# Kernel optimization log

Measured on AMD Instinct MI355X. Metric: run time of the kernel, lower is better.

Reference implementation:

```python
import jax, jax.numpy as jnp
import numpy as np

H = 256; EMB = 256; MAX_POS = 20; NBOND = 4; ATOM = 40
DEPTH_T = 5; DEPTH_G = 5
NT, MT = 8000, 16000      # tree nodes / tree messages
NA, MA = 25000, 50000     # atoms / bond messages
NB = 6; NC = 12; NROOT = 256
VC, VI = 5000, 15000      # cluster / inter vocab sizes

FLOAT_KEYS = ("E_c","E_i","Wc_w","Wc_b","Wi_w","Wi_b","Wroot_w","Wroot_b",
  "t_Wo_w","t_Wo_b","t_Wz_w","t_Wz_b","t_Wr_w","t_Ur_w","t_Ur_b","t_Wh_w","t_Wh_b",
  "i_Wo_w","i_Wo_b","i_Wz_w","i_Wz_b","i_Wr_w","i_Ur_w","i_Ur_b","i_Wh_w","i_Wh_b",
  "g_Wo_w","g_Wo_b","g_Wz_w","g_Wz_b","g_Wr_w","g_Ur_w","g_Ur_b","g_Wh_w","g_Wh_b")
INT_KEYS = ("t_fnode","t_fmess","t_agraph","t_bgraph","t_cgraph",
            "g_fnode","g_fmess","g_agraph","g_bgraph","roots")

def _gru(fmess, bgraph, Wz_w, Wz_b, Wr_w, Ur_w, Ur_b, Wh_w, Wh_b, depth):
    # depth-iterated GRU message passing; row 0 of h is padding (kept at zero).
    M, F = fmess.shape
    Hs = Wz_w.shape[1]
    mask = jnp.ones((M, 1), fmess.dtype).at[0, 0].set(0.0)
    # loop-invariant input projections (W_z/W_h split along concat axis)
    fz = fmess @ Wz_w[:F] + Wz_b
    fr = fmess @ Wr_w
    fh = fmess @ Wh_w[:F] + Wh_b
    Wz_h, Wh_h = Wz_w[F:], Wh_w[F:]
    def step(h, _):
        h_nei = h[bgraph]                       # [M, B, H] irregular gather
        sum_h = h_nei.sum(1)
        z = jax.nn.sigmoid(fz + sum_h @ Wz_h)
        r = jax.nn.sigmoid(fr[:, None, :] + h_nei @ Ur_w + Ur_b)
        sum_gh = (r * h_nei).sum(1)
        pre_h = jnp.tanh(fh + sum_gh @ Wh_h)
        h_new = ((1.0 - z) * sum_h + z * pre_h) * mask
        return h_new, None
    h0 = jnp.zeros((M, Hs), fmess.dtype)
    h, _ = jax.lax.scan(step, h0, None, length=depth)
    return h

def _mpn(fnode, fmess, agraph, bgraph, p, depth):
    h = _gru(fmess, bgraph, p["Wz_w"], p["Wz_b"], p["Wr_w"], p["Ur_w"], p["Ur_b"], p["Wh_w"], p["Wh_b"], depth)
    nei = h[agraph].sum(1)                      # index_select_ND + sum
    nh = jax.nn.relu(jnp.concatenate([fnode, nei], 1) @ p["Wo_w"] + p["Wo_b"])
    return nh.at[0].set(0.0), h                 # zero padding row (mask)

def _enc_params(fl, pre):
    return {k: fl[pre + k] for k in ("Wo_w","Wo_b","Wz_w","Wz_b","Wr_w","Ur_w","Ur_b","Wh_w","Wh_b")}

def _forward(fl, it):
    E_pos = jnp.eye(MAX_POS, dtype=jnp.float32)
    E_a = jnp.eye(ATOM, dtype=jnp.float32)
    E_b = jnp.eye(NBOND, dtype=jnp.float32)
    t_fnode, t_fmess = it["t_fnode"], it["t_fmess"]
    g_fnode, g_fmess = it["g_fnode"], it["g_fmess"]
    # ---- embed_graph + graph_encoder ----
    g_hnode = E_a[g_fnode]                                           # [NA, ATOM] one-hot
    g_hmess = jnp.concatenate([g_hnode[g_fmess[:, 0]], E_b[g_fmess[:, 2]], E_pos[g_fmess[:, 3]]], 1)
    hatom, _ = _mpn(g_hnode, g_hmess, it["g_agraph"], it["g_bgraph"], _enc_params(fl, "g_"), DEPTH_G)
    # ---- embed_inter + inter_encoder ----
    fin = fl["E_i"][t_fnode[:, 1]]
    hn = hatom[it["t_cgraph"]].sum(1)                                # cluster <- atoms
    hn = jax.nn.relu(jnp.concatenate([fin, hn], 1) @ fl["Wi_w"] + fl["Wi_b"])
    hm = jnp.concatenate([hn[t_fmess[:, 0]], E_pos[t_fmess[:, 2]]], 1)
    hinter, _ = _mpn(hn, hm, it["t_agraph"], it["t_bgraph"], _enc_params(fl, "i_"), DEPTH_T)
    # ---- embed_tree + tree_encoder ----
    fin = fl["E_c"][t_fnode[:, 0]]
    hn = jax.nn.relu(jnp.concatenate([fin, hinter], 1) @ fl["Wc_w"] + fl["Wc_b"])
    hm = jnp.concatenate([hn[t_fmess[:, 0]], E_pos[t_fmess[:, 2]]], 1)
    htree, h_msg = _mpn(hn, hm, it["t_agraph"], it["t_bgraph"], _enc_params(fl, "t_"), DEPTH_T)
    # ---- embed_root: uses pre-encoder node embedding hn and message states h_msg ----
    r = it["roots"]
    nei = h_msg[it["t_agraph"][r]].sum(1)
    hroot = jnp.tanh(jnp.concatenate([hn[r], nei], 1) @ fl["Wroot_w"] + fl["Wroot_b"])
    return hroot, htree, hinter, hatom

def setup_inputs() -> dict:
    ki = iter(jax.random.split(jax.random.key(0), 80))
    def nk():
        return next(ki)
    ri = jax.random.randint
    rn = lambda shape: 0.08 * jax.random.normal(nk(), shape, jnp.float32)
    inp = {}
    inp["t_fnode"] = ri(nk(), (NT, 2), 0, VC)
    inp["t_fmess"] = jnp.stack([ri(nk(), (MT,), 0, NT), ri(nk(), (MT,), 0, NT), ri(nk(), (MT,), 0, MAX_POS)], 1)
    inp["t_agraph"] = ri(nk(), (NT, NB), 0, MT)
    inp["t_bgraph"] = ri(nk(), (MT, NB), 0, MT)
    inp["t_cgraph"] = ri(nk(), (NT, NC), 0, NA)
    inp["g_fnode"] = ri(nk(), (NA,), 0, ATOM)
    inp["g_fmess"] = jnp.stack([ri(nk(), (MA,), 0, NA), ri(nk(), (MA,), 0, NA), ri(nk(), (MA,), 0, NBOND), ri(nk(), (MA,), 0, MAX_POS)], 1)
    inp["g_agraph"] = ri(nk(), (NA, NB), 0, MA)
    inp["g_bgraph"] = ri(nk(), (MA, NB), 0, MA)
    inp["roots"] = ri(nk(), (NROOT,), 0, NT)
    inp["E_c"] = rn((VC, EMB)); inp["E_i"] = rn((VI, EMB))
    inp["Wc_w"] = rn((EMB + H, H)); inp["Wc_b"] = rn((H,))
    inp["Wi_w"] = rn((EMB + H, H)); inp["Wi_b"] = rn((H,))
    inp["Wroot_w"] = rn((2 * H, H)); inp["Wroot_b"] = rn((H,))
    for pre, in_sz, nf in (("t_", H + MAX_POS, H), ("i_", H + MAX_POS, H), ("g_", ATOM + NBOND + MAX_POS, ATOM)):
        inp[pre + "Wo_w"] = rn((nf + H, H)); inp[pre + "Wo_b"] = rn((H,))
        inp[pre + "Wz_w"] = rn((in_sz + H, H)); inp[pre + "Wz_b"] = rn((H,))
        inp[pre + "Wr_w"] = rn((in_sz, H))
        inp[pre + "Ur_w"] = rn((H, H)); inp[pre + "Ur_b"] = rn((H,))
        inp[pre + "Wh_w"] = rn((in_sz + H, H)); inp[pre + "Wh_b"] = rn((H,))
    return inp

def reference(E_c, E_i, Wc_w, Wc_b, Wi_w, Wi_b, Wroot_w, Wroot_b,
              t_Wo_w, t_Wo_b, t_Wz_w, t_Wz_b, t_Wr_w, t_Ur_w, t_Ur_b, t_Wh_w, t_Wh_b,
              i_Wo_w, i_Wo_b, i_Wz_w, i_Wz_b, i_Wr_w, i_Ur_w, i_Ur_b, i_Wh_w, i_Wh_b,
              g_Wo_w, g_Wo_b, g_Wz_w, g_Wz_b, g_Wr_w, g_Ur_w, g_Ur_b, g_Wh_w, g_Wh_b,
              t_fnode, t_fmess, t_agraph, t_bgraph, t_cgraph,
              g_fnode, g_fmess, g_agraph, g_bgraph, roots):
    a = dict(locals())
    fl = {k: a[k] for k in FLOAT_KEYS}
    it = {k: a[k] for k in INT_KEYS}
    return _forward(fl, it)
```

## Files before the change

kernel.cpp:

```cpp
#include <hip/hip_runtime.h>
#include <hip/hip_bf16.h>
#include <math.h>

typedef __hip_bfloat16 bf16;
typedef __attribute__((ext_vector_type(8))) short  bf16x8;
typedef __attribute__((ext_vector_type(4))) float  f32x4;

#define NT_ 8000
#define MT_ 16000
#define NA_ 25000
#define MA_ 50000
#define NROOT_ 256

struct Feat {
  const float* dtab; const int* didx; int dstride;
  const float* otab;
  const int* oidx0; int os0; int oo0;
  const int* oidx1; int os1; int oo1;
  const int* oidx2; int os2; int oo2;
  const float* bias;
};

__device__ __forceinline__ float rcpf_(float x){ return __builtin_amdgcn_rcpf(x); }
__device__ __forceinline__ float sigm(float x){ return rcpf_(1.0f + __expf(-x)); }
__device__ __forceinline__ float tanh_f(float x){
  float t = __expf(2.0f*x);
  return 1.0f - 2.0f*rcpf_(t + 1.0f);
}

__device__ __forceinline__ float ubf(unsigned int u){ union{unsigned int i; float f;} x; x.i = u<<16; return x.f; }
__device__ __forceinline__ unsigned int pack2bf(float a, float b){
  bf16 x = __float2bfloat16(a), y = __float2bfloat16(b);
  unsigned short ux = *(unsigned short*)&x, uy = *(unsigned short*)&y;
  return (unsigned int)ux | ((unsigned int)uy<<16);
}
__device__ __forceinline__ short f2bf_s(float f){
  bf16 b = __float2bfloat16(f);
  return *(short*)&b;
}
__device__ __forceinline__ float bfs2f(short s){ return ubf((unsigned short)s); }

__device__ __forceinline__ void acc4(float4& v, const float* p){
  float4 t = *(const float4*)p;
  v.x+=t.x; v.y+=t.y; v.z+=t.z; v.w+=t.w;
}
__device__ __forceinline__ float4 feat_eval4(const Feat& f, int m, int n){
  float4 v = make_float4(0,0,0,0);
  if (f.bias) acc4(v, f.bias + n);
  if (f.dtab) acc4(v, f.dtab + (size_t)f.didx[(size_t)m*f.dstride]*256 + n);
  if (f.otab){
    acc4(v, f.otab + (size_t)(f.oidx0[(size_t)m*f.os0]+f.oo0)*256 + n);
    if (f.oidx1) acc4(v, f.otab + (size_t)(f.oidx1[(size_t)m*f.os1]+f.oo1)*256 + n);
    if (f.oidx2) acc4(v, f.otab + (size_t)(f.oidx2[(size_t)m*f.os2]+f.oo2)*256 + n);
  }
  return v;
}
__device__ __forceinline__ float feat_eval(const Feat& f, int m, int n){
  float v = 0.0f;
  if (f.bias) v += f.bias[n];
  if (f.dtab) v += f.dtab[(size_t)f.didx[(size_t)m*f.dstride]*256 + n];
  if (f.otab){
    v += f.otab[((size_t)(f.oidx0[(size_t)m*f.os0]+f.oo0))*256 + n];
    if (f.oidx1) v += f.otab[((size_t)(f.oidx1[(size_t)m*f.os1]+f.oo1))*256 + n];
    if (f.oidx2) v += f.otab[((size_t)(f.oidx2[(size_t)m*f.os2]+f.oo2))*256 + n];
  }
  return v;
}

__global__ void k_aidx(const int* __restrict__ g_fnode, const int* __restrict__ g_fmess,
                       int* __restrict__ aidx, int M){
  int m = blockIdx.x*blockDim.x + threadIdx.x;
  if (m<M) aidx[m] = g_fnode[g_fmess[(size_t)m*4]];
}

struct SJob { const float* src; short* dst; int nrow; int pad; };
struct SJobs { SJob j[26]; };
__global__ void k_splitw_b(SJobs js){
  SJob jb = js.j[blockIdx.y];
  int idx = blockIdx.x*256 + threadIdx.x;
  if (idx >= jb.nrow*256) return;
  int k = idx>>8, n = idx&255;
  float w = jb.src[idx];
  int base = (((k>>5)*16 + (n>>4))<<10) + (((n&15) + (((k>>3)&3)<<4))<<4) + (k&7);
  short h = f2bf_s(w);
  jb.dst[base]   = h;
  jb.dst[base+8] = f2bf_s(w - bfs2f(h));
}

__global__ void k_gsum4(const float* __restrict__ src, const int* __restrict__ idx,
                        const int* __restrict__ rowsel, int J, int istride,
                        float* __restrict__ dst, int M){
  int wid = (blockIdx.x<<2) + (threadIdx.x>>6);
  if (wid>=M) return;
  int c = (threadIdx.x&63)<<2;
  int r = rowsel ? rowsel[wid] : wid;
  float4 s = make_float4(0,0,0,0);
  for (int j=0;j<J;j++){
    int id = idx[(size_t)r*istride+j];
    acc4(s, src + (size_t)id*256 + c);
  }
  *(float4*)(dst + (size_t)wid*256 + c) = s;
}

__device__ __forceinline__ void build_a(const float* p, bf16x8& hi, bf16x8& lo){
  float4 v0 = *(const float4*)p;
  float4 v1 = *(const float4*)(p+4);
  float vv[8]={v0.x,v0.y,v0.z,v0.w,v1.x,v1.y,v1.z,v1.w};
  #pragma unroll
  for (int j=0;j<8;j++){
    short h = f2bf_s(vv[j]);
    hi[j]=h;
    lo[j]=f2bf_s(vv[j]-bfs2f(h));
  }
}

#define MFMA __builtin_amdgcn_mfma_f32_16x16x32_bf16
#define PRIO_HI __builtin_amdgcn_s_setprio(1)
#define PRIO_LO __builtin_amdgcn_s_setprio(0)

__global__ __launch_bounds__(256)
void mfma_mm(const float* __restrict__ A, const short* __restrict__ Bp,
             float* __restrict__ outf, int M)
{
  const int tid=threadIdx.x, lane=tid&63, wc=tid>>6;
  const int rbase = blockIdx.x<<5;
  const int r0 = rbase + (lane&15), r1 = r0 + 16;
  const int koff = (lane>>4)<<3;
  f32x4 zero = {0.f,0.f,0.f,0.f};
  f32x4 acc[2][4];
  #pragma unroll
  for (int rf=0;rf<2;rf++)
    #pragma unroll
    for (int t=0;t<4;t++) acc[rf][t]=zero;

  PRIO_HI;
  for (int kc=0;kc<8;kc++){
    bf16x8 a0h={0,0,0,0,0,0,0,0}, a0l=a0h, a1h=a0h, a1l=a0h;
    if (r0<M) build_a(A + (size_t)r0*256 + kc*32 + koff, a0h, a0l);
    if (r1<M) build_a(A + (size_t)r1*256 + kc*32 + koff, a1h, a1l);
    #pragma unroll
    for (int t=0;t<4;t++){
      const short* p = Bp + (((kc<<4)+(wc<<2)+t)<<10) + (lane<<4);
      bf16x8 bh = *(const bf16x8*)p;
      bf16x8 bl = *(const bf16x8*)(p+8);
      acc[0][t]=MFMA(a0h,bh,acc[0][t],0,0,0);
      acc[1][t]=MFMA(a1h,bh,acc[1][t],0,0,0);
      acc[0][t]=MFMA(a0l,bh,acc[0][t],0,0,0);
      acc[1][t]=MFMA(a1l,bh,acc[1][t],0,0,0);
      acc[0][t]=MFMA(a0h,bl,acc[0][t],0,0,0);
      acc[1][t]=MFMA(a1h,bl,acc[1][t],0,0,0);
    }
  }
  PRIO_LO;
  const int rr = rbase + ((lane>>4)<<2);
  const int cl = lane&15;
  #pragma unroll
  for (int rf=0;rf<2;rf++)
    #pragma unroll
    for (int t=0;t<4;t++){
      int col = (((wc<<2)+t)<<4) + cl;
      #pragma unroll
      for (int r=0;r<4;r++){
        int m = rr + rf*16 + r;
        if (m<M) outf[(size_t)m*256+col] = acc[rf][t][r];
      }
    }
}

template<int NG>
__global__ __launch_bounds__(256)
void mfma_proj(const float* __restrict__ A1, const int* __restrict__ a1idx, int a1s,
               const float* __restrict__ A2,
               const short* __restrict__ B1p, const short* __restrict__ B2p,
               float* __restrict__ outf, float* __restrict__ outf2,
               Feat f1, int mask0, int M)
{
  const int tid=threadIdx.x, lane=tid&63, wc=tid>>6;
  const int rbase = blockIdx.x<<5;
  const int r0 = rbase + (lane&15), r1 = r0 + 16;
  const int koff = (lane>>4)<<3;
  const float* p0 = (r0<M) ? A1 + (size_t)(a1idx? a1idx[(size_t)r0*a1s] : r0)*256 : nullptr;
  const float* p1 = (r1<M) ? A1 + (size_t)(a1idx? a1idx[(size_t)r1*a1s] : r1)*256 : nullptr;
  f32x4 zero = {0.f,0.f,0.f,0.f};
  f32x4 acc[2][4];
  #pragma unroll
  for (int rf=0;rf<2;rf++)
    #pragma unroll
    for (int t=0;t<4;t++) acc[rf][t]=zero;

  PRIO_HI;
  for (int kc=0;kc<8;kc++){
    bf16x8 a0h={0,0,0,0,0,0,0,0}, a0l=a0h, a1h=a0h, a1l=a0h;
    bf16x8 c0h=a0h, c0l=a0h, c1h=a0h, c1l=a0h;
    if (p0) build_a(p0 + kc*32 + koff, a0h, a0l);
    if (p1) build_a(p1 + kc*32 + koff, a1h, a1l);
    if (NG==2){
      if (r0<M) build_a(A2 + (size_t)r0*256 + kc*32 + koff, c0h, c0l);
      if (r1<M) build_a(A2 + (size_t)r1*256 + kc*32 + koff, c1h, c1l);
    }
    #pragma unroll
    for (int t=0;t<4;t++){
      const short* p = B1p + (((kc<<4)+(wc<<2)+t)<<10) + (lane<<4);
      bf16x8 bh = *(const bf16x8*)p;
      bf16x8 bl = *(const bf16x8*)(p+8);
      acc[0][t]=MFMA(a0h,bh,acc[0][t],0,0,0);
      acc[1][t]=MFMA(a1h,bh,acc[1][t],0,0,0);
      acc[0][t]=MFMA(a0l,bh,acc[0][t],0,0,0);
      acc[1][t]=MFMA(a1l,bh,acc[1][t],0,0,0);
      acc[0][t]=MFMA(a0h,bl,acc[0][t],0,0,0);
      acc[1][t]=MFMA(a1h,bl,acc[1][t],0,0,0);
      if (NG==2){
        const short* q = B2p + (((kc<<4)+(wc<<2)+t)<<10) + (lane<<4);
        bf16x8 dh = *(const bf16x8*)q;
        bf16x8 dl = *(const bf16x8*)(q+8);
        acc[0][t]=MFMA(c0h,dh,acc[0][t],0,0,0);
        acc[1][t]=MFMA(c1h,dh,acc[1][t],0,0,0);
        acc[0][t]=MFMA(c0l,dh,acc[0][t],0,0,0);
        acc[1][t]=MFMA(c1l,dh,acc[1][t],0,0,0);
        acc[0][t]=MFMA(c0h,dl,acc[0][t],0,0,0);
        acc[1][t]=MFMA(c1h,dl,acc[1][t],0,0,0);
      }
    }
  }
  PRIO_LO;
  const int rr = rbase + ((lane>>4)<<2);
  const int cl = lane&15;
  #pragma unroll
  for (int rf=0;rf<2;rf++)
    #pragma unroll
    for (int t=0;t<4;t++){
      int col = (((wc<<2)+t)<<4) + cl;
      #pragma unroll
      for (int r=0;r<4;r++){
        int m = rr + rf*16 + r;
        if (m>=M) continue;
        float v = acc[rf][t][r] + feat_eval(f1, m, col);
        v = fmaxf(v, 0.0f);
        if (mask0 && m==0) v = 0.0f;
        outf[(size_t)m*256+col] = v;
        if (outf2) outf2[(size_t)m*256+col] = v;
      }
    }
}

__global__ __launch_bounds__(256)
void k_step1hu(Feat fz, Feat fh, const short* __restrict__ Bu,
               float* __restrict__ hout, bf16* __restrict__ hUout, int M)
{
  __shared__ short Hs[32][264];
  const int tid=threadIdx.x, lane=tid&63, wc=tid>>6;
  const int rbase = blockIdx.x<<5;
  const int rr = (lane>>4)<<2;
  const int cl = lane&15;
  const int koff = (lane>>4)<<3;

  #pragma unroll
  for (int rf=0;rf<2;rf++)
    #pragma unroll
    for (int t=0;t<4;t++){
      int col = (((wc<<2)+t)<<4) + cl;
      #pragma unroll
      for (int r=0;r<4;r++){
        int lrow = rr + rf*16 + r;
        int m = rbase + lrow;
        float v = 0.f;
        if (m<M && m!=0)
          v = sigm(feat_eval(fz,m,col))*tanh_f(feat_eval(fh,m,col));
        if (m<M) hout[(size_t)m*256+col]=v;
        Hs[lrow][col]=f2bf_s(v);
      }
    }
  __syncthreads();
  const int r0l = lane&15, r1l = r0l+16;
  f32x4 zero = {0.f,0.f,0.f,0.f};
  f32x4 acc[2][4];
  #pragma unroll
  for (int rf=0;rf<2;rf++)
    #pragma unroll
    for (int t=0;t<4;t++) acc[rf][t]=zero;
  PRIO_HI;
  for (int kc=0;kc<8;kc++){
    bf16x8 a0 = *(const bf16x8*)&Hs[r0l][kc*32+koff];
    bf16x8 a1 = *(const bf16x8*)&Hs[r1l][kc*32+koff];
    #pragma unroll
    for (int t=0;t<4;t++){
      const short* p = Bu + (((kc<<4)+(wc<<2)+t)<<10) + (lane<<4);
      bf16x8 bh = *(const bf16x8*)p;
      bf16x8 bl = *(const bf16x8*)(p+8);
      acc[0][t]=MFMA(a0,bh,acc[0][t],0,0,0);
      acc[1][t]=MFMA(a1,bh,acc[1][t],0,0,0);
      acc[0][t]=MFMA(a0,bl,acc[0][t],0,0,0);
      acc[1][t]=MFMA(a1,bl,acc[1][t],0,0,0);
    }
  }
  PRIO_LO;
  #pragma unroll
  for (int rf=0;rf<2;rf++)
    #pragma unroll
    for (int t=0;t<4;t++){
      int col = (((wc<<2)+t)<<4) + cl;
      #pragma unroll
      for (int r=0;r<4;r++){
        int m = rbase + rr + rf*16 + r;
        if (m<M) hUout[(size_t)m*256+col] = __float2bfloat16(acc[rf][t][r]);
      }
    }
}

template<int GEXT, int DO_HU>
__global__ __launch_bounds__(256)
void mfma_gg(const float* __restrict__ hprev, const bf16* __restrict__ hUprev,
             const int* __restrict__ bgraph, Feat fr,
             const short* __restrict__ Bz, const short* __restrict__ Bh,
             const short* __restrict__ Bze, const short* __restrict__ Bhe,
             const int* __restrict__ aidx, const int* __restrict__ gfm,
             const float* __restrict__ bzb, const float* __restrict__ bhb,
             Feat fz, Feat fh, const short* __restrict__ Bu,
             float* __restrict__ hout, bf16* __restrict__ hUout, int M)
{
  __shared__ float SH[32][260];
  __shared__ short SG[32][264];
  const int tid=threadIdx.x, lane=tid&63, wc=tid>>6;
  const int rbase = blockIdx.x<<5;
  const int koff = (lane>>4)<<3;

  {
    const int c = lane<<2;
    #pragma unroll 2
    for (int s=0;s<8;s++){
      int lrow = (wc<<3) + s;
      int m = rbase + lrow;
      float4 sv = make_float4(0,0,0,0);
      float4 gv = make_float4(0,0,0,0);
      if (m < M){
        float4 fr4 = feat_eval4(fr, m, c);
        const int* bg = bgraph + (size_t)m*6;
        #pragma unroll
        for (int j=0;j<6;j++){
          int id = bg[j];
          float4 h4 = *(const float4*)(hprev + (size_t)id*256 + c);
          uint2  u2 = *(const uint2*)(hUprev + (size_t)id*256 + c);
          float u0=ubf(u2.x&0xffffu), u1=ubf(u2.x>>16);
          float u2f=ubf(u2.y&0xffffu), u3=ubf(u2.y>>16);
          sv.x+=h4.x; sv.y+=h4.y; sv.z+=h4.z; sv.w+=h4.w;
          gv.x += sigm(fr4.x+u0 )*h4.x;
          gv.y += sigm(fr4.y+u1 )*h4.y;
          gv.z += sigm(fr4.z+u2f)*h4.z;
          gv.w += sigm(fr4.w+u3 )*h4.w;
        }
      }
      *(float4*)&SH[lrow][c] = sv;
      uint2 p; p.x = pack2bf(gv.x,gv.y); p.y = pack2bf(gv.z,gv.w);
      *(uint2*)&SG[lrow][c] = p;
    }
  }
  __syncthreads();

  const int r0l = lane&15, r1l = r0l+16;
  const int r0 = rbase + r0l, r1 = rbase + r1l;
  f32x4 zero = {0.f,0.f,0.f,0.f};
  f32x4 accz[2][4], acch[2][4];
  #pragma unroll
  for (int rf=0;rf<2;rf++)
    #pragma unroll
    for (int t=0;t<4;t++){ accz[rf][t]=zero; acch[rf][t]=zero; }

  PRIO_HI;
  for (int kc=0;kc<8;kc++){
    bf16x8 a0h, a0l, a1h, a1l;
    build_a(&SH[r0l][kc*32+koff], a0h, a0l);
    build_a(&SH[r1l][kc*32+koff], a1h, a1l);
    bf16x8 s0 = *(const bf16x8*)&SG[r0l][kc*32+koff];
    bf16x8 s1 = *(const bf16x8*)&SG[r1l][kc*32+koff];
    #pragma unroll
    for (int t=0;t<4;t++){
      const short* pz = Bz + (((kc<<4)+(wc<<2)+t)<<10) + (lane<<4);
      const short* ph = Bh + (((kc<<4)+(wc<<2)+t)<<10) + (lane<<4);
      bf16x8 bzh = *(const bf16x8*)pz;
      bf16x8 bzl = *(const bf16x8*)(pz+8);
      bf16x8 bhh = *(const bf16x8*)ph;
      bf16x8 bhl = *(const bf16x8*)(ph+8);
      accz[0][t]=MFMA(a0h,bzh,accz[0][t],0,0,0);
      accz[1][t]=MFMA(a1h,bzh,accz[1][t],0,0,0);
      accz[0][t]=MFMA(a0l,bzh,accz[0][t],0,0,0);
      accz[1][t]=MFMA(a1l,bzh,accz[1][t],0,0,0);
      accz[0][t]=MFMA(a0h,bzl,accz[0][t],0,0,0);
      accz[1][t]=MFMA(a1h,bzl,accz[1][t],0,0,0);
      acch[0][t]=MFMA(s0,bhh,acch[0][t],0,0,0);
      acch[1][t]=MFMA(s1,bhh,acch[1][t],0,0,0);
      acch[0][t]=MFMA(s0,bhl,acch[0][t],0,0,0);
      acch[1][t]=MFMA(s1,bhl,acch[1][t],0,0,0);
    }
  }

  if (GEXT){
    int h0a=-1,h0b=-1,h0c=-1,h1a=-1,h1b=-1,h1c=-1;
    if (r0<M){ h0a=aidx[r0]; h0b=40+gfm[(size_t)r0*4+2]; h0c=44+gfm[(size_t)r0*4+3]; }
    if (r1<M){ h1a=aidx[r1]; h1b=40+gfm[(size_t)r1*4+2]; h1c=44+gfm[(size_t)r1*4+3]; }
    #pragma unroll
    for (int e=0;e<2;e++){
      bf16x8 ax0, ax1;
      #pragma unroll
      for (int j=0;j<8;j++){
        int d = e*32 + koff + j;
        ax0[j] = (d==h0a||d==h0b||d==h0c) ? (short)0x3F80 : (short)0;
        ax1[j] = (d==h1a||d==h1b||d==h1c) ? (short)0x3F80 : (short)0;
      }
      #pragma unroll
      for (int t=0;t<4;t++){
        const short* pe = Bze + (((e<<4)+(wc<<2)+t)<<10) + (lane<<4);
        const short* qe = Bhe + (((e<<4)+(wc<<2)+t)<<10) + (lane<<4);
        bf16x8 bzeh = *(const bf16x8*)pe;
        bf16x8 bzel = *(const bf16x8*)(pe+8);
        bf16x8 bheh = *(const bf16x8*)qe;
        bf16x8 bhel = *(const bf16x8*)(qe+8);
        accz[0][t]=MFMA(ax0,bzeh,accz[0][t],0,0,0);
        accz[1][t]=MFMA(ax1,bzeh,accz[1][t],0,0,0);
        accz[0][t]=MFMA(ax0,bzel,accz[0][t],0,0,0);
        accz[1][t]=MFMA(ax1,bzel,accz[1][t],0,0,0);
        acch[0][t]=MFMA(ax0,bheh,acch[0][t],0,0,0);
        acch[1][t]=MFMA(ax1,bheh,acch[1][t],0,0,0);
        acch[0][t]=MFMA(ax0,bhel,acch[0][t],0,0,0);
        acch[1][t]=MFMA(ax1,bhel,acch[1][t],0,0,0);
      }
    }
  }
  PRIO_LO;

  __syncthreads();

  const int rr = (lane>>4)<<2;
  const int cl = lane&15;
  int src8[8], pos8[8];
  if (!GEXT){
    #pragma unroll
    for (int rf=0;rf<2;rf++)
      #pragma unroll
      for (int r=0;r<4;r++){
        int m = rbase + rr + rf*16 + r;
        int mm = (m<M)? m : 0;
        src8[rf*4+r] = fz.didx [(size_t)mm*fz.dstride];
        pos8[rf*4+r] = fz.oidx0[(size_t)mm*fz.os0] + fz.oo0;
      }
  }
  #pragma unroll
  for (int rf=0;rf<2;rf++)
    #pragma unroll
    for (int t=0;t<4;t++){
      int col = (((wc<<2)+t)<<4) + cl;
      float fzb=0.f, fhb=0.f;
      if (GEXT){ fzb = bzb[col]; fhb = bhb[col]; }
      #pragma unroll
      for (int r=0;r<4;r++){
        int lrow = rr + rf*16 + r;
        int m = rbase + lrow;
        float v = 0.f;
        if (m<M){
          float fzv, fhv;
          if (GEXT){ fzv = fzb; fhv = fhb; }
          else {
            int i8 = rf*4+r;
            size_t so = (size_t)src8[i8]*256 + col;
            size_t po = (size_t)pos8[i8]*256 + col;
            fzv = fz.bias[col] + fz.dtab[so] + fz.otab[po];
            fhv = fh.bias[col] + fh.dtab[so] + fh.otab[po];
          }
          float z   = sigm  (accz[rf][t][r] + fzv);
          float pre = tanh_f(acch[rf][t][r] + fhv);
          float sh  = SH[lrow][col];
          v = (m==0) ? 0.f : ((1.f-z)*sh + z*pre);
          hout[(size_t)m*256+col] = v;
        }
        if (DO_HU) SG[lrow][col] = f2bf_s(v);
      }
    }

  if (DO_HU){
    __syncthreads();
    f32x4 acc[2][4];
    #pragma unroll
    for (int rf=0;rf<2;rf++)
      #pragma unroll
      for (int t=0;t<4;t++) acc[rf][t]=zero;
    PRIO_HI;
    for (int kc=0;kc<8;kc++){
      bf16x8 a0 = *(const bf16x8*)&SG[r0l][kc*32+koff];
      bf16x8 a1 = *(const bf16x8*)&SG[r1l][kc*32+koff];
      #pragma unroll
      for (int t=0;t<4;t++){
        const short* p = Bu + (((kc<<4)+(wc<<2)+t)<<10) + (lane<<4);
        bf16x8 bh = *(const bf16x8*)p;
        bf16x8 bl = *(const bf16x8*)(p+8);
        acc[0][t]=MFMA(a0,bh,acc[0][t],0,0,0);
        acc[1][t]=MFMA(a1,bh,acc[1][t],0,0,0);
        acc[0][t]=MFMA(a0,bl,acc[0][t],0,0,0);
        acc[1][t]=MFMA(a1,bl,acc[1][t],0,0,0);
      }
    }
    PRIO_LO;
    #pragma unroll
    for (int rf=0;rf<2;rf++)
      #pragma unroll
      for (int t=0;t<4;t++){
        int col = (((wc<<2)+t)<<4) + cl;
        #pragma unroll
        for (int r=0;r<4;r++){
          int m = rbase + rr + rf*16 + r;
          if (m<M) hUout[(size_t)m*256+col] = __float2bfloat16(acc[rf][t][r]);
        }
      }
  }
}

template<int NG, int MODE>
__global__ __launch_bounds__(256)
void gemm256(const float* __restrict__ A1, const float* __restrict__ B1,
             const float* __restrict__ A2, const float* __restrict__ B2,
             float* __restrict__ Cf, int M, Feat f1, int mask0)
{
  __shared__ float As[NG][16][36];
  __shared__ float Bs[NG][16][260];
  const int tid = threadIdx.x;
  const int bm = blockIdx.x<<5;
  const int tm = (tid>>5)<<2;
  const int c0 = (tid&31)<<2;

  float acc[NG][4][8];
  #pragma unroll
  for (int g=0;g<NG;g++)
    #pragma unroll
    for (int i=0;i<4;i++)
      #pragma unroll
      for (int j=0;j<8;j++) acc[g][i][j]=0.f;

  const int t7  = tid & 127;
  const int alm = t7>>2;
  const int alk = (t7&3)<<2;
  const int arow = bm + alm;
  const int amat = (NG==2)? (tid>>7) : 0;
  const bool astage = (NG==2) || (tid<128);

  for (int k0=0;k0<256;k0+=16){
    float a0=0,a1=0,a2=0,a3=0;
    if (astage && arow<M){
      const float* src = (amat==0)? A1 : A2;
      float4 v = *(const float4*)(src + (size_t)arow*256 + k0 + alk);
      a0=v.x; a1=v.y; a2=v.z; a3=v.w;
    }
    float4 breg[NG][4];
    #pragma unroll
    for (int g=0; g<NG; g++){
      const float* B = (g==0)? B1 : B2;
      #pragma unroll
      for (int j=0;j<4;j++){
        int slot = tid + 256*j;
        int kb = slot>>6, nb = (slot&63)<<2;
        breg[g][j] = *(const float4*)(B + (size_t)(k0+kb)*256 + nb);
      }
    }
    __syncthreads();
    if (astage){
      As[amat][alk+0][alm]=a0; As[amat][alk+1][alm]=a1;
      As[amat][alk+2][alm]=a2; As[amat][alk+3][alm]=a3;
    }
    #pragma unroll
    for (int g=0; g<NG; g++){
      #pragma unroll
      for (int j=0;j<4;j++){
        int slot = tid + 256*j;
        int kb = slot>>6, nb = (slot&63)<<2;
        *(float4*)&Bs[g][kb][nb] = breg[g][j];
      }
    }
    __syncthreads();
    #pragma unroll
    for (int k=0;k<16;k++){
      #pragma unroll
      for (int g=0;g<NG;g++){
        float4 av = *(const float4*)&As[g][k][tm];
        float4 b0 = *(const float4*)&Bs[g][k][c0];
        float4 b1 = *(const float4*)&Bs[g][k][c0+128];
        float a_[4]={av.x,av.y,av.z,av.w};
        float b_[8]={b0.x,b0.y,b0.z,b0.w,b1.x,b1.y,b1.z,b1.w};
        #pragma unroll
        for (int i=0;i<4;i++)
          #pragma unroll
          for (int j=0;j<8;j++)
            acc[g][i][j] = fmaf(a_[i], b_[j], acc[g][i][j]);
      }
    }
  }

  #pragma unroll
  for (int i=0;i<4;i++){
    int m = bm + tm + i;
    if (m >= M) continue;
    #pragma unroll
    for (int half=0; half<2; half++){
      int c = c0 + half*128;
      float4 r;
      float* rr = &r.x;
      float4 ft = feat_eval4(f1, m, c);
      float fv[4]={ft.x,ft.y,ft.z,ft.w};
      #pragma unroll
      for (int j=0;j<4;j++){
        float s = acc[0][i][half*4+j] + (NG>1?acc[1][i][half*4+j]:0.f) + fv[j];
        float v = (MODE==1)? fmaxf(s,0.f) : tanhf(s);
        if (MODE==1 && mask0 && m==0) v = 0.f;
        rr[j] = v;
      }
      *(float4*)(Cf + (size_t)m*256+c) = r;
    }
  }
}

extern "C" void kernel_launch(void* const* d_in, const int* in_sizes, int n_in,
                              void* d_out, int out_size, void* d_ws, size_t ws_size,
                              hipStream_t stream)
{
  const int* t_fnode  = (const int*)d_in[0];
  const int* t_fmess  = (const int*)d_in[1];
  const int* t_agraph = (const int*)d_in[2];
  const int* t_bgraph = (const int*)d_in[3];
  const int* t_cgraph = (const int*)d_in[4];
  const int* g_fnode  = (const int*)d_in[5];
  const int* g_fmess  = (const int*)d_in[6];
  const int* g_agraph = (const int*)d_in[7];
  const int* g_bgraph = (const int*)d_in[8];
  const int* roots    = (const int*)d_in[9];
  const float* E_c     = (const float*)d_in[10];
  const float* E_i     = (const float*)d_in[11];
  const float* Wc_w    = (const float*)d_in[12];
  const float* Wc_b    = (const float*)d_in[13];
  const float* Wi_w    = (const float*)d_in[14];
  const float* Wi_b    = (const float*)d_in[15];
  const float* Wroot_w = (const float*)d_in[16];
  const float* Wroot_b = (const float*)d_in[17];
  const float* t_Wo_w  = (const float*)d_in[18];
  const float* t_Wo_b  = (const float*)d_in[19];
  const float* t_Wz_w  = (const float*)d_in[20];
  const float* t_Wz_b  = (const float*)d_in[21];
  const float* t_Wr_w  = (const float*)d_in[22];
  const float* t_Ur_w  = (const float*)d_in[23];
  const float* t_Ur_b  = (const float*)d_in[24];
  const float* t_Wh_w  = (const float*)d_in[25];
  const float* t_Wh_b  = (const float*)d_in[26];
  const float* i_Wo_w  = (const float*)d_in[27];
  const float* i_Wo_b  = (const float*)d_in[28];
  const float* i_Wz_w  = (const float*)d_in[29];
  const float* i_Wz_b  = (const float*)d_in[30];
  const float* i_Wr_w  = (const float*)d_in[31];
  const float* i_Ur_w  = (const float*)d_in[32];
  const float* i_Ur_b  = (const float*)d_in[33];
  const float* i_Wh_w  = (const float*)d_in[34];
  const float* i_Wh_b  = (const float*)d_in[35];
  const float* g_Wo_w  = (const float*)d_in[36];
  const float* g_Wo_b  = (const float*)d_in[37];
  const float* g_Wz_w  = (const float*)d_in[38];
  const float* g_Wz_b  = (const float*)d_in[39];
  const float* g_Wr_w  = (const float*)d_in[40];
  const float* g_Ur_w  = (const float*)d_in[41];
  const float* g_Ur_b  = (const float*)d_in[42];
  const float* g_Wh_w  = (const float*)d_in[43];
  const float* g_Wh_b  = (const float*)d_in[44];

  float* out        = (float*)d_out;
  float* out_hroot  = out;
  float* out_htree  = out + (size_t)65536;
  float* out_hinter = out + (size_t)65536 + 2048000;
  float* out_hatom  = out + (size_t)65536 + 2048000 + 2048000;

  char* base = (char*)d_ws;
  int*   aidx   = (int*)base;
  short* SP     = (short*)(base + 262144);
  float* hbuf   = (float*)(base + 262144 + 8388608);
  float* hbufB  = hbuf + (size_t)12800000;
  bf16*  hUbuf  = (bf16*)(hbufB + (size_t)12800000);
  bf16*  hUbufB = hUbuf + (size_t)12800000;

  auto GP = [&](int i)->short* { return SP + (size_t)i*131072; };
  short* EZ = SP + (size_t)9*131072;
  short* EH = EZ + 32768;
  auto HP = [&](int j)->short* { return EH + 32768 + (size_t)j*131072; };
  short* P2 = EH + 32768 + (size_t)6*131072;
  auto PP = [&](int j)->short* { return P2 + (size_t)j*131072; };

  float* neibG    = hbufB;
  float* hatom    = hbufB + (size_t)25000*256;
  float* neib_t   = hbuf;
  float* hn_i     = hbuf  + (size_t)16000*256;
  float* hnWz     = hbufB + (size_t)16000*256;
  float* hnWr     = hbufB + (size_t)24000*256;
  float* hnWh     = hbufB + (size_t)32000*256;
  float* nei_i    = hbufB;
  float* hinter   = hbufB + (size_t)8000*256;
  float* hn_t     = hbuf  + (size_t)32000*256;
  float* nei_t    = hbufB;
  float* hn_roots = hbufB + (size_t)8000*256;
  float* nei_root = hbufB + (size_t)8256*256;

  (void)in_sizes; (void)n_in; (void)out_size; (void)ws_size;

  SJobs js;
  js.j[0]  = { g_Ur_w,                    GP(0), 256, 0 };
  js.j[1]  = { g_Wz_w + (size_t)64*256,   GP(1), 256, 0 };
  js.j[2]  = { g_Wh_w + (size_t)64*256,   GP(2), 256, 0 };
  js.j[3]  = { i_Ur_w,                    GP(3), 256, 0 };
  js.j[4]  = { i_Wz_w + (size_t)276*256,  GP(4), 256, 0 };
  js.j[5]  = { i_Wh_w + (size_t)276*256,  GP(5), 256, 0 };
  js.j[6]  = { t_Ur_w,                    GP(6), 256, 0 };
  js.j[7]  = { t_Wz_w + (size_t)276*256,  GP(7), 256, 0 };
  js.j[8]  = { t_Wh_w + (size_t)276*256,  GP(8), 256, 0 };
  js.j[9]  = { g_Wz_w,                    EZ,     64, 0 };
  js.j[10] = { g_Wh_w,                    EH,     64, 0 };
  js.j[11] = { i_Wz_w,                    HP(0), 256, 0 };
  js.j[12] = { i_Wr_w,                    HP(1), 256, 0 };
  js.j[13] = { i_Wh_w,                    HP(2), 256, 0 };
  js.j[14] = { t_Wz_w,                    HP(3), 256, 0 };
  js.j[15] = { t_Wr_w,                    HP(4), 256, 0 };
  js.j[16] = { t_Wh_w,                    HP(5), 256, 0 };
  js.j[17] = { Wi_w,                      PP(0), 256, 0 };
  js.j[18] = { Wi_w + (size_t)256*256,    PP(1), 256, 0 };
  js.j[19] = { Wc_w,                      PP(2), 256, 0 };
  js.j[20] = { Wc_w + (size_t)256*256,    PP(3), 256, 0 };
  js.j[21] = { i_Wo_w,                    PP(4), 256, 0 };
  js.j[22] = { i_Wo_w + (size_t)256*256,  PP(5), 256, 0 };
  js.j[23] = { t_Wo_w,                    PP(6), 256, 0 };
  js.j[24] = { t_Wo_w + (size_t)256*256,  PP(7), 256, 0 };
  js.j[25] = { g_Wo_w + (size_t)40*256,   PP(8), 256, 0 };
  k_splitw_b<<<dim3(256,26),256,0,stream>>>(js);

  Feat fzg{}; fzg.otab=g_Wz_w; fzg.oidx0=aidx;      fzg.os0=1; fzg.oo0=0;
              fzg.oidx1=g_fmess+2; fzg.os1=4; fzg.oo1=40;
              fzg.oidx2=g_fmess+3; fzg.os2=4; fzg.oo2=44; fzg.bias=g_Wz_b;
  Feat frg = fzg; frg.otab=g_Wr_w; frg.bias=g_Ur_b;
  Feat fhg = fzg; fhg.otab=g_Wh_w; fhg.bias=g_Wh_b;

  Feat fzi{}; fzi.dtab=hnWz; fzi.didx=t_fmess; fzi.dstride=3;
              fzi.otab=i_Wz_w; fzi.oidx0=t_fmess+2; fzi.os0=3; fzi.oo0=256; fzi.bias=i_Wz_b;
  Feat fri = fzi; fri.dtab=hnWr; fri.otab=i_Wr_w; fri.bias=i_Ur_b;
  Feat fhi = fzi; fhi.dtab=hnWh; fhi.otab=i_Wh_w; fhi.bias=i_Wh_b;

  Feat fzt = fzi; fzt.otab=t_Wz_w; fzt.bias=t_Wz_b;
  Feat frt = fri; frt.otab=t_Wr_w; frt.bias=t_Ur_b;
  Feat fht = fhi; fht.otab=t_Wh_w; fht.bias=t_Wh_b;

  Feat fnone{};

  auto run_gru = [&](int M, const int* bgraph, int p, bool gext,
                     Feat fz, Feat fr, Feat fh)->float* {
    int gb32 = (M+31)/32;
    const short* Bu = GP(p*3+0);
    const short* Bz = GP(p*3+1);
    const short* Bh = GP(p*3+2);
    k_step1hu<<<gb32,256,0,stream>>>(fz, fh, Bu, hbuf, hUbuf, M);
    float* hA = hbuf;  bf16* uA = hUbuf;
    float* hB = hbufB; bf16* uB = hUbufB;
    for (int d=0; d<4; ++d){
      if (d<3){
        if (gext)
          mfma_gg<1,1><<<gb32,256,0,stream>>>(hA, uA, bgraph, fr, Bz, Bh,
              EZ, EH, aidx, g_fmess, g_Wz_b, g_Wh_b, fnone, fnone, Bu, hB, uB, M);
        else
          mfma_gg<0,1><<<gb32,256,0,stream>>>(hA, uA, bgraph, fr, Bz, Bh,
              nullptr,nullptr,nullptr,nullptr,nullptr,nullptr, fz, fh, Bu, hB, uB, M);
      } else {
        if (gext)
          mfma_gg<1,0><<<gb32,256,0,stream>>>(hA, uA, bgraph, fr, Bz, Bh,
              EZ, EH, aidx, g_fmess, g_Wz_b, g_Wh_b, fnone, fnone, nullptr, hB, nullptr, M);
        else
          mfma_gg<0,0><<<gb32,256,0,stream>>>(hA, uA, bgraph, fr, Bz, Bh,
              nullptr,nullptr,nullptr,nullptr,nullptr,nullptr, fz, fh, nullptr, hB, nullptr, M);
      }
      float* th=hA; hA=hB; hB=th;
      bf16*  tu=uA; uA=uB; uB=tu;
    }
    return hA;
  };

  k_aidx<<<(MA_+255)/256,256,0,stream>>>(g_fnode, g_fmess, aidx, MA_);
  float* hg = run_gru(MA_, g_bgraph, 0, true, fzg, frg, fhg);
  k_gsum4<<<(NA_+3)/4,256,0,stream>>>(hg, g_agraph, nullptr, 6, 6, neibG, NA_);
  Feat fWo{}; fWo.otab=g_Wo_w; fWo.oidx0=g_fnode; fWo.os0=1; fWo.oo0=0; fWo.bias=g_Wo_b;
  mfma_proj<1><<<(NA_+31)/32,256,0,stream>>>(neibG, nullptr, 1, nullptr,
      PP(8), nullptr, hatom, out_hatom, fWo, 1, NA_);

  k_gsum4<<<(NT_+3)/4,256,0,stream>>>(hatom, t_cgraph, nullptr, 12, 12, neib_t, NT_);
  Feat fbWi{}; fbWi.bias=Wi_b;
  mfma_proj<2><<<NT_/32,256,0,stream>>>(E_i, t_fnode+1, 2, neib_t,
      PP(0), PP(1), hn_i, nullptr, fbWi, 0, NT_);
  mfma_mm<<<NT_/32,256,0,stream>>>(hn_i, HP(0), hnWz, NT_);
  mfma_mm<<<NT_/32,256,0,stream>>>(hn_i, HP(1), hnWr, NT_);
  mfma_mm<<<NT_/32,256,0,stream>>>(hn_i, HP(2), hnWh, NT_);

  float* hi = run_gru(MT_, t_bgraph, 1, false, fzi, fri, fhi);
  k_gsum4<<<(NT_+3)/4,256,0,stream>>>(hi, t_agraph, nullptr, 6, 6, nei_i, NT_);
  Feat fbWoi{}; fbWoi.bias=i_Wo_b;
  mfma_proj<2><<<NT_/32,256,0,stream>>>(hn_i, nullptr, 1, nei_i,
      PP(4), PP(5), hinter, out_hinter, fbWoi, 1, NT_);

  Feat fbWc{}; fbWc.bias=Wc_b;
  mfma_proj<2><<<NT_/32,256,0,stream>>>(E_c, t_fnode, 2, hinter,
      PP(2), PP(3), hn_t, nullptr, fbWc, 0, NT_);
  mfma_mm<<<NT_/32,256,0,stream>>>(hn_t, HP(3), hnWz, NT_);
  mfma_mm<<<NT_/32,256,0,stream>>>(hn_t, HP(4), hnWr, NT_);
  mfma_mm<<<NT_/32,256,0,stream>>>(hn_t, HP(5), hnWh, NT_);

  float* ht = run_gru(MT_, t_bgraph, 2, false, fzt, frt, fht);
  k_gsum4<<<(NT_+3)/4,256,0,stream>>>(ht, t_agraph, nullptr, 6, 6, nei_t, NT_);
  Feat fbWot{}; fbWot.bias=t_Wo_b;
  mfma_proj<2><<<NT_/32,256,0,stream>>>(hn_t, nullptr, 1, nei_t,
      PP(6), PP(7), out_htree, nullptr, fbWot, 1, NT_);

  k_gsum4<<<(NROOT_+3)/4,256,0,stream>>>(hn_t, roots, nullptr, 1, 1, hn_roots, NROOT_);
  k_gsum4<<<(NROOT_+3)/4,256,0,stream>>>(ht, t_agraph, roots, 6, 6, nei_root, NROOT_);
  Feat fbWr{}; fbWr.bias=Wroot_b;
  gemm256<2,2><<<NROOT_/32,256,0,stream>>>(hn_roots, Wroot_w, nei_root,
      Wroot_w + (size_t)256*256, out_hroot, NROOT_, fbWr, 0);
}
```

Measured before the change: 1.858 ms.

## Pack GRU hidden state as fp16 with bf16 hU into one interleaved record

```diff
diff --git a/kernel.cpp b/kernel.cpp
--- a/kernel.cpp
+++ b/kernel.cpp
@@ -1,5 +1,6 @@
 #include <hip/hip_runtime.h>
 #include <hip/hip_bf16.h>
+#include <hip/hip_fp16.h>
 #include <math.h>
 
 typedef __hip_bfloat16 bf16;
@@ -29,16 +30,15 @@
 }
 
 __device__ __forceinline__ float ubf(unsigned int u){ union{unsigned int i; float f;} x; x.i = u<<16; return x.f; }
-__device__ __forceinline__ unsigned int pack2bf(float a, float b){
-  bf16 x = __float2bfloat16(a), y = __float2bfloat16(b);
-  unsigned short ux = *(unsigned short*)&x, uy = *(unsigned short*)&y;
-  return (unsigned int)ux | ((unsigned int)uy<<16);
-}
 __device__ __forceinline__ short f2bf_s(float f){
   bf16 b = __float2bfloat16(f);
   return *(short*)&b;
 }
 __device__ __forceinline__ float bfs2f(short s){ return ubf((unsigned short)s); }
+__device__ __forceinline__ float rec_h(unsigned int u){
+  return __half2float(__ushort_as_half((unsigned short)(u>>16)));
+}
+__device__ __forceinline__ float rec_u(unsigned int u){ return ubf(u&0xffffu); }
 
 __device__ __forceinline__ void acc4(float4& v, const float* p){
   float4 t = *(const float4*)p;
@@ -245,7 +245,7 @@
 
 __global__ __launch_bounds__(256)
 void k_step1hu(Feat fz, Feat fh, const short* __restrict__ Bu,
-               float* __restrict__ hout, bf16* __restrict__ hUout, int M)
+               unsigned int* __restrict__ recout, int M)
 {
   __shared__ short Hs[32][264];
   const int tid=threadIdx.x, lane=tid&63, wc=tid>>6;
@@ -253,6 +253,7 @@
   const int rr = (lane>>4)<<2;
   const int cl = lane&15;
   const int koff = (lane>>4)<<3;
+  unsigned short hreg[32];
 
   #pragma unroll
   for (int rf=0;rf<2;rf++)
@@ -266,8 +267,8 @@
         float v = 0.f;
         if (m<M && m!=0)
           v = sigm(feat_eval(fz,m,col))*tanh_f(feat_eval(fh,m,col));
-        if (m<M) hout[(size_t)m*256+col]=v;
         Hs[lrow][col]=f2bf_s(v);
+        hreg[(((rf<<2)+t)<<2)+r] = __half_as_ushort(__float2half(v));
       }
     }
   __syncthreads();
@@ -302,21 +303,25 @@
       #pragma unroll
       for (int r=0;r<4;r++){
         int m = rbase + rr + rf*16 + r;
-        if (m<M) hUout[(size_t)m*256+col] = __float2bfloat16(acc[rf][t][r]);
+        if (m<M){
+          unsigned int hw = hreg[(((rf<<2)+t)<<2)+r];
+          unsigned int uw = (unsigned short)f2bf_s(acc[rf][t][r]);
+          recout[(size_t)m*256+col] = (hw<<16) | uw;
+        }
       }
     }
 }
 
 template<int GEXT, int DO_HU>
 __global__ __launch_bounds__(256)
-void mfma_gg(const float* __restrict__ hprev, const bf16* __restrict__ hUprev,
+void mfma_gg(const unsigned int* __restrict__ recprev,
              const int* __restrict__ bgraph, Feat fr,
              const short* __restrict__ Bz, const short* __restrict__ Bh,
              const short* __restrict__ Bze, const short* __restrict__ Bhe,
              const int* __restrict__ aidx, const int* __restrict__ gfm,
              const float* __restrict__ bzb, const float* __restrict__ bhb,
              Feat fz, Feat fh, const short* __restrict__ Bu,
-             float* __restrict__ hout, bf16* __restrict__ hUout, int M)
+             unsigned int* __restrict__ recout, float* __restrict__ houtF, int M)
 {
   __shared__ float SH[32][260];
   __shared__ short SG[32][264];
@@ -338,19 +343,20 @@
         #pragma unroll
         for (int j=0;j<6;j++){
           int id = bg[j];
-          float4 h4 = *(const float4*)(hprev + (size_t)id*256 + c);
-          uint2  u2 = *(const uint2*)(hUprev + (size_t)id*256 + c);
-          float u0=ubf(u2.x&0xffffu), u1=ubf(u2.x>>16);
-          float u2f=ubf(u2.y&0xffffu), u3=ubf(u2.y>>16);
-          sv.x+=h4.x; sv.y+=h4.y; sv.z+=h4.z; sv.w+=h4.w;
-          gv.x += sigm(fr4.x+u0 )*h4.x;
-          gv.y += sigm(fr4.y+u1 )*h4.y;
-          gv.z += sigm(fr4.z+u2f)*h4.z;
-          gv.w += sigm(fr4.w+u3 )*h4.w;
+          uint4 u = *(const uint4*)(recprev + (size_t)id*256 + c);
+          float h0=rec_h(u.x), h1=rec_h(u.y), h2=rec_h(u.z), h3=rec_h(u.w);
+          float u0=rec_u(u.x), u1=rec_u(u.y), u2f=rec_u(u.z), u3=rec_u(u.w);
+          sv.x+=h0; sv.y+=h1; sv.z+=h2; sv.w+=h3;
+          gv.x += sigm(fr4.x+u0 )*h0;
+          gv.y += sigm(fr4.y+u1 )*h1;
+          gv.z += sigm(fr4.z+u2f)*h2;
+          gv.w += sigm(fr4.w+u3 )*h3;
         }
       }
       *(float4*)&SH[lrow][c] = sv;
-      uint2 p; p.x = pack2bf(gv.x,gv.y); p.y = pack2bf(gv.z,gv.w);
+      uint2 p;
+      p.x = ((unsigned int)(unsigned short)f2bf_s(gv.y)<<16) | (unsigned short)f2bf_s(gv.x);
+      p.y = ((unsigned int)(unsigned short)f2bf_s(gv.w)<<16) | (unsigned short)f2bf_s(gv.z);
       *(uint2*)&SG[lrow][c] = p;
     }
   }
@@ -431,6 +437,7 @@
 
   const int rr = (lane>>4)<<2;
   const int cl = lane&15;
+  unsigned short hreg[32];
   int src8[8], pos8[8];
   if (!GEXT){
     #pragma unroll
@@ -469,9 +476,12 @@
           float pre = tanh_f(acch[rf][t][r] + fhv);
           float sh  = SH[lrow][col];
           v = (m==0) ? 0.f : ((1.f-z)*sh + z*pre);
-          hout[(size_t)m*256+col] = v;
+          if (!DO_HU) houtF[(size_t)m*256+col] = v;
         }
-        if (DO_HU) SG[lrow][col] = f2bf_s(v);
+        if (DO_HU){
+          SG[lrow][col] = f2bf_s(v);
+          hreg[(((rf<<2)+t)<<2)+r] = __half_as_ushort(__float2half(v));
+        }
       }
     }
 
@@ -506,7 +516,11 @@
         #pragma unroll
         for (int r=0;r<4;r++){
           int m = rbase + rr + rf*16 + r;
-          if (m<M) hUout[(size_t)m*256+col] = __float2bfloat16(acc[rf][t][r]);
+          if (m<M){
+            unsigned int hw = hreg[(((rf<<2)+t)<<2)+r];
+            unsigned int uw = (unsigned short)f2bf_s(acc[rf][t][r]);
+            recout[(size_t)m*256+col] = (hw<<16) | uw;
+          }
         }
       }
   }
@@ -671,12 +685,13 @@
   float* out_hatom  = out + (size_t)65536 + 2048000 + 2048000;
 
   char* base = (char*)d_ws;
-  int*   aidx   = (int*)base;
-  short* SP     = (short*)(base + 262144);
-  float* hbuf   = (float*)(base + 262144 + 8388608);
-  float* hbufB  = hbuf + (size_t)12800000;
-  bf16*  hUbuf  = (bf16*)(hbufB + (size_t)12800000);
-  bf16*  hUbufB = hUbuf + (size_t)12800000;
+  int*   aidx  = (int*)base;
+  short* SP    = (short*)(base + 262144);
+  float* W0    = (float*)(base + 262144 + 8388608);
+  unsigned int* R0 = (unsigned int*)(W0 + (size_t)12800000);
+  unsigned int* R1 = R0 + (size_t)12800000;
+  float* R0f = (float*)R0;
+  float* R1f = (float*)R1;
 
   auto GP = [&](int i)->short* { return SP + (size_t)i*131072; };
   short* EZ = SP + (size_t)9*131072;
@@ -685,19 +700,19 @@
   short* P2 = EH + 32768 + (size_t)6*131072;
   auto PP = [&](int j)->short* { return P2 + (size_t)j*131072; };
 
-  float* neibG    = hbufB;
-  float* hatom    = hbufB + (size_t)25000*256;
-  float* neib_t   = hbuf;
-  float* hn_i     = hbuf  + (size_t)16000*256;
-  float* hnWz     = hbufB + (size_t)16000*256;
-  float* hnWr     = hbufB + (size_t)24000*256;
-  float* hnWh     = hbufB + (size_t)32000*256;
-  float* nei_i    = hbufB;
-  float* hinter   = hbufB + (size_t)8000*256;
-  float* hn_t     = hbuf  + (size_t)32000*256;
-  float* nei_t    = hbufB;
-  float* hn_roots = hbufB + (size_t)8000*256;
-  float* nei_root = hbufB + (size_t)8256*256;
+  float* neibG    = R0f;
+  float* hatom    = R1f;
+  float* neib_t   = R0f;
+  float* hn_i     = W0 + (size_t)16000*256;
+  float* hnWz     = W0 + (size_t)24000*256;
+  float* hnWr     = W0 + (size_t)32000*256;
+  float* hnWh     = W0 + (size_t)40000*256;
+  float* nei_i    = R0f;
+  float* hinter   = R1f;
+  float* hn_t     = W0 + (size_t)16000*256;
+  float* nei_t    = R0f;
+  float* hn_roots = R1f;
+  float* nei_root = R1f + (size_t)256*256;
 
   (void)in_sizes; (void)n_in; (void)out_size; (void)ws_size;
 
@@ -753,29 +768,28 @@
     const short* Bu = GP(p*3+0);
     const short* Bz = GP(p*3+1);
     const short* Bh = GP(p*3+2);
-    k_step1hu<<<gb32,256,0,stream>>>(fz, fh, Bu, hbuf, hUbuf, M);
-    float* hA = hbuf;  bf16* uA = hUbuf;
-    float* hB = hbufB; bf16* uB = hUbufB;
+    k_step1hu<<<gb32,256,0,stream>>>(fz, fh, Bu, R0, M);
+    unsigned int* rA = R0;
+    unsigned int* rB = R1;
     for (int d=0; d<4; ++d){
       if (d<3){
         if (gext)
-          mfma_gg<1,1><<<gb32,256,0,stream>>>(hA, uA, bgraph, fr, Bz, Bh,
-              EZ, EH, aidx, g_fmess, g_Wz_b, g_Wh_b, fnone, fnone, Bu, hB, uB, M);
+          mfma_gg<1,1><<<gb32,256,0,stream>>>(rA, bgraph, fr, Bz, Bh,
+              EZ, EH, aidx, g_fmess, g_Wz_b, g_Wh_b, fnone, fnone, Bu, rB, nullptr, M);
         else
-          mfma_gg<0,1><<<gb32,256,0,stream>>>(hA, uA, bgraph, fr, Bz, Bh,
-              nullptr,nullptr,nullptr,nullptr,nullptr,nullptr, fz, fh, Bu, hB, uB, M);
+          mfma_gg<0,1><<<gb32,256,0,stream>>>(rA, bgraph, fr, Bz, Bh,
+              nullptr,nullptr,nullptr,nullptr,nullptr,nullptr, fz, fh, Bu, rB, nullptr, M);
       } else {
         if (gext)
-          mfma_gg<1,0><<<gb32,256,0,stream>>>(hA, uA, bgraph, fr, Bz, Bh,
-              EZ, EH, aidx, g_fmess, g_Wz_b, g_Wh_b, fnone, fnone, nullptr, hB, nullptr, M);
+          mfma_gg<1,0><<<gb32,256,0,stream>>>(rA, bgraph, fr, Bz, Bh,
+              EZ, EH, aidx, g_fmess, g_Wz_b, g_Wh_b, fnone, fnone, nullptr, nullptr, W0, M);
         else
-          mfma_gg<0,0><<<gb32,256,0,stream>>>(hA, uA, bgraph, fr, Bz, Bh,
-              nullptr,nullptr,nullptr,nullptr,nullptr,nullptr, fz, fh, nullptr, hB, nullptr, M);
-      }
-      float* th=hA; hA=hB; hB=th;
-      bf16*  tu=uA; uA=uB; uB=tu;
-    }
-    return hA;
+          mfma_gg<0,0><<<gb32,256,0,stream>>>(rA, bgraph, fr, Bz, Bh,
+              nullptr,nullptr,nullptr,nullptr,nullptr,nullptr, fz, fh, nullptr, nullptr, W0, M);
+      }
+      unsigned int* t=rA; rA=rB; rB=t;
+    }
+    return W0;
   };
 
   k_aidx<<<(MA_+255)/256,256,0,stream>>>(g_fnode, g_fmess, aidx, MA_);
```

Result: faster. 1.784 ms (-4.0%).
